# Performance work log

Measured on AMD Instinct MI355X. Metric: run time of the kernel, lower is better.

Reference implementation:

```python
import jax, jax.numpy as jnp
import numpy as np


def log_g(x):
    # log of g(x) = x+0.5 if x>=0 else sigmoid(x)
    return jnp.where(x >= 0, jnp.log(jax.nn.relu(x) + 0.5), -jax.nn.softplus(-x))


def setup_inputs() -> dict:
    key = jax.random.key(0)
    B, T, D, H = 8, 4096, 1024, 1024
    ks = jax.random.split(key, 7)
    s = 1.0 / np.sqrt(D)
    return {
        "x": jax.random.normal(ks[0], (B, T, D), dtype=jnp.float32),
        "h0": jnp.zeros((B, 1, H), dtype=jnp.float32),
        "W_f": jax.random.uniform(ks[1], (H, D), jnp.float32, -s, s),
        "b_f": jax.random.uniform(ks[2], (H,), jnp.float32, -s, s),
        "W_i": jax.random.uniform(ks[3], (H, D), jnp.float32, -s, s),
        "b_i": jax.random.uniform(ks[4], (H,), jnp.float32, -s, s),
        "W_h": jax.random.uniform(ks[5], (H, D), jnp.float32, -s, s),
        "b_h": jax.random.uniform(ks[6], (H,), jnp.float32, -s, s),
    }


def reference(x, h0, W_f, b_f, W_i, b_i, W_h, b_h):
    # gate pre-activations: [B, T, H]
    zf = jnp.einsum("btd,hd->bth", x, W_f) + b_f
    zi = jnp.einsum("btd,hd->bth", x, W_i) + b_i
    zh = jnp.einsum("btd,hd->bth", x, W_h) + b_h
    diff = jax.nn.softplus(-zf) - jax.nn.softplus(-zi)
    log_f = -jax.nn.softplus(diff)        # log f'_t
    log_i = -jax.nn.softplus(-diff)       # log i'_t
    log_values = jnp.concatenate([log_g(h0), log_i + log_g(zh)], axis=1)  # [B, T+1, H]
    # parallel scan in log space
    a_star = jnp.pad(jnp.cumsum(log_f, axis=1), ((0, 0), (1, 0), (0, 0)))  # [B, T+1, H]
    log_h = a_star + jax.lax.cumlogsumexp(log_values - a_star, axis=1)
    return jnp.exp(log_h)[:, 1:]  # [B, T, H]
```

## Files before the change

### kernel.cpp

```cpp
#include <hip/hip_runtime.h>
#include <hip/hip_bf16.h>
#include <stdint.h>
#include <stddef.h>

#define B_ 8
#define T_ 4096
#define D_ 1024
#define H_ 1024
#define M_ (B_*T_)
#define N_ 3072
#define K_ 1024
#define CHUNK 64
#define NCHUNK 64
#define NWG ((M_/256)*(N_/256))

typedef __attribute__((ext_vector_type(8))) __bf16 bf16v8;
typedef __attribute__((ext_vector_type(4))) float f32x4;
typedef __attribute__((ext_vector_type(8))) unsigned short u16x8;

#define REG_SZ 16384
#define SLOT_SZ 32768
#define BOFF 65536
#define LDS_BYTES 131072

#define FENCE() asm volatile("" ::: "memory")
#define SBAR()  __builtin_amdgcn_s_barrier()

__device__ __forceinline__ unsigned short f2bf(float f) {
  union { float f; unsigned u; } x; x.f = f;
  return (unsigned short)((x.u + 0x7fffu + ((x.u >> 16) & 1u)) >> 16);
}

__global__ __launch_bounds__(256) void cvt_x(const float* __restrict__ src,
                                             unsigned short* __restrict__ dst) {
  int i = blockIdx.x * 256 + threadIdx.x;
  const float4* s = (const float4*)src;
  float4 a = s[i*2], b = s[i*2+1];
  u16x8 o;
  o[0]=f2bf(a.x); o[1]=f2bf(a.y); o[2]=f2bf(a.z); o[3]=f2bf(a.w);
  o[4]=f2bf(b.x); o[5]=f2bf(b.y); o[6]=f2bf(b.z); o[7]=f2bf(b.w);
  *(u16x8*)(dst + (size_t)i*8) = o;
}

__global__ __launch_bounds__(256) void cvt_w(const float* __restrict__ w0,
                                             const float* __restrict__ w1,
                                             const float* __restrict__ w2,
                                             unsigned short* __restrict__ dst) {
  int i = blockIdx.x * 256 + threadIdx.x;
  int seg = i >> 17;
  int off = i & 131071;
  const float* src = (seg == 0) ? w0 : (seg == 1) ? w1 : w2;
  const float4* s = (const float4*)src;
  float4 a = s[off*2], b = s[off*2+1];
  u16x8 o;
  o[0]=f2bf(a.x); o[1]=f2bf(a.y); o[2]=f2bf(a.z); o[3]=f2bf(a.w);
  o[4]=f2bf(b.x); o[5]=f2bf(b.y); o[6]=f2bf(b.z); o[7]=f2bf(b.w);
  *(u16x8*)(dst + (size_t)i*8) = o;
}

__device__ __forceinline__ void stage_half(int k, int m0, int n0,
    const unsigned short* Abf, const unsigned short* Bbf, char* smem, int tid) {
  if (k > 63) return;
  int t = k >> 2, w = k & 3;
  int q   = (w >= 2) ? 1 : 0;
  int isA = (w == 0 || w == 3);
  int slot = t & 1;
  int k0 = t * 64;
  const unsigned short* gbase = isA ? (Abf + (size_t)(m0 + q*128) * K_)
                                    : (Bbf + (size_t)(n0 + q*128) * K_);
  char* lbase = smem + (isA ? 0 : BOFF) + slot*SLOT_SZ + q*REG_SZ;
  #pragma unroll
  for (int l = 0; l < 2; ++l) {
    int o = tid*16 + l*8192;
    int row = o >> 7, cb = o & 127;
    int scb = cb ^ ((row & 7) << 4);
    const unsigned short* g = gbase + (size_t)row * K_ + k0 + (scb >> 1);
    __builtin_amdgcn_global_load_lds((const __attribute__((address_space(1))) void*)g,
        (__attribute__((address_space(3))) void*)(lbase + o), 16, 0, 0);
  }
}

__device__ __forceinline__ bf16v8 ldsA(const char* smem, int slot, int q, int rr, int cb) {
  return *(const bf16v8*)(smem + slot*SLOT_SZ + q*REG_SZ + rr*128 + (cb ^ ((rr & 7) << 4)));
}
__device__ __forceinline__ bf16v8 ldsB(const char* smem, int slot, int q, int rr, int cb) {
  return *(const bf16v8*)(smem + BOFF + slot*SLOT_SZ + q*REG_SZ + rr*128 + (cb ^ ((rr & 7) << 4)));
}

__global__ __launch_bounds__(512, 2) void gemm_gates(
    const unsigned short* __restrict__ Abf,
    const unsigned short* __restrict__ Bbf,
    const float* __restrict__ bf_, const float* __restrict__ bi_,
    const float* __restrict__ bh_,
    float* __restrict__ zf, float* __restrict__ zi, float* __restrict__ zh)
{
  extern __shared__ char smem[];
  int tid = threadIdx.x;
  int bid = blockIdx.x;
  int swz = (bid & 7) * (NWG/8) + (bid >> 3);
  int tn = swz % 12, tm = swz / 12;
  int m0 = tm*256, n0 = tn*256;
  int lane = tid & 63, wid = tid >> 6;
  int wm = wid >> 2, wn = wid & 3;
  int lr = lane & 15, lhi = lane >> 4;
  int cbL = lhi * 16;

  f32x4 acc[8][4] = {};
  bf16v8 a0[4][2], b0[2][2], b1[2][2];

  #pragma unroll
  for (int k = 0; k < 7; ++k) stage_half(k, m0, n0, Abf, Bbf, smem, tid);
  asm volatile("s_waitcnt vmcnt(6)" ::: "memory");
  SBAR(); FENCE();

  for (int t = 0; t < 16; ++t) {
    int slot = t & 1;
    #pragma unroll
    for (int i = 0; i < 4; ++i)
      #pragma unroll
      for (int kk = 0; kk < 2; ++kk)
        a0[i][kk] = ldsA(smem, slot, 0, wm*64 + i*16 + lr, kk*64 + cbL);
    #pragma unroll
    for (int j = 0; j < 2; ++j)
      #pragma unroll
      for (int kk = 0; kk < 2; ++kk)
        b0[j][kk] = ldsB(smem, slot, 0, wn*32 + j*16 + lr, kk*64 + cbL);
    stage_half(4*t + 7, m0, n0, Abf, Bbf, smem, tid);
    FENCE(); SBAR(); FENCE();
    __builtin_amdgcn_s_setprio(1);
    #pragma unroll
    for (int i = 0; i < 4; ++i)
      #pragma unroll
      for (int j = 0; j < 2; ++j)
        #pragma unroll
        for (int kk = 0; kk < 2; ++kk)
          acc[i][j] = __builtin_amdgcn_mfma_f32_16x16x32_bf16(a0[i][kk], b0[j][kk], acc[i][j], 0, 0, 0);
    __builtin_amdgcn_s_setprio(0);
    FENCE(); SBAR(); FENCE();
    #pragma unroll
    for (int j = 0; j < 2; ++j)
      #pragma unroll
      for (int kk = 0; kk < 2; ++kk)
        b1[j][kk] = ldsB(smem, slot, 1, wn*32 + j*16 + lr, kk*64 + cbL);
    stage_half(4*t + 8, m0, n0, Abf, Bbf, smem, tid);
    FENCE(); SBAR(); FENCE();
    __builtin_amdgcn_s_setprio(1);
    #pragma unroll
    for (int i = 0; i < 4; ++i)
      #pragma unroll
      for (int j = 0; j < 2; ++j)
        #pragma unroll
        for (int kk = 0; kk < 2; ++kk)
          acc[i][2+j] = __builtin_amdgcn_mfma_f32_16x16x32_bf16(a0[i][kk], b1[j][kk], acc[i][2+j], 0, 0, 0);
    __builtin_amdgcn_s_setprio(0);
    FENCE(); SBAR(); FENCE();
    #pragma unroll
    for (int i = 0; i < 4; ++i)
      #pragma unroll
      for (int kk = 0; kk < 2; ++kk)
        a0[i][kk] = ldsA(smem, slot, 1, wm*64 + i*16 + lr, kk*64 + cbL);
    stage_half(4*t + 9, m0, n0, Abf, Bbf, smem, tid);
    FENCE(); SBAR(); FENCE();
    __builtin_amdgcn_s_setprio(1);
    #pragma unroll
    for (int i = 0; i < 4; ++i)
      #pragma unroll
      for (int j = 0; j < 2; ++j)
        #pragma unroll
        for (int kk = 0; kk < 2; ++kk)
          acc[4+i][2+j] = __builtin_amdgcn_mfma_f32_16x16x32_bf16(a0[i][kk], b1[j][kk], acc[4+i][2+j], 0, 0, 0);
    __builtin_amdgcn_s_setprio(0);
    FENCE(); SBAR(); FENCE();
    stage_half(4*t + 10, m0, n0, Abf, Bbf, smem, tid);
    FENCE(); SBAR(); FENCE();
    __builtin_amdgcn_s_setprio(1);
    #pragma unroll
    for (int i = 0; i < 4; ++i)
      #pragma unroll
      for (int j = 0; j < 2; ++j)
        #pragma unroll
        for (int kk = 0; kk < 2; ++kk)
          acc[4+i][j] = __builtin_amdgcn_mfma_f32_16x16x32_bf16(a0[i][kk], b0[j][kk], acc[4+i][j], 0, 0, 0);
    __builtin_amdgcn_s_setprio(0);
    if (t < 14) { asm volatile("s_waitcnt vmcnt(6)" ::: "memory"); }
    else        { asm volatile("s_waitcnt vmcnt(0)" ::: "memory"); }
    SBAR(); FENCE();
  }

  int g = n0 >> 10;
  float* Z = (g == 0) ? zf : (g == 1) ? zi : zh;
  const float* bias = (g == 0) ? bf_ : (g == 1) ? bi_ : bh_;
  int ncol0 = n0 & 1023;
  #pragma unroll
  for (int qm = 0; qm < 2; ++qm)
    #pragma unroll
    for (int i = 0; i < 4; ++i)
      #pragma unroll
      for (int qn = 0; qn < 2; ++qn)
        #pragma unroll
        for (int j = 0; j < 2; ++j) {
          int col = ncol0 + qn*128 + wn*32 + j*16 + lr;
          float bv = bias[col];
          int row = m0 + qm*128 + wm*64 + i*16 + lhi*4;
          f32x4 a = acc[qm*4+i][qn*2+j];
          #pragma unroll
          for (int r = 0; r < 4; ++r)
            Z[(size_t)(row + r)*H_ + col] = a[r] + bv;
        }
}

__device__ __forceinline__ void gate_eval(float vzf, float vzi, float vzh,
                                          float& f, float& v) {
  float spf = fmaxf(-vzf, 0.f) + __logf(1.f + __expf(-fabsf(vzf)));
  float spi = fmaxf(-vzi, 0.f) + __logf(1.f + __expf(-fabsf(vzi)));
  float d   = spf - spi;
  float l1  = __logf(1.f + __expf(-fabsf(d)));
  f = __expf(-(fmaxf(d, 0.f) + l1));
  float iv = __expf(-(fmaxf(-d, 0.f) + l1));
  float gv = (vzh >= 0.f) ? (vzh + 0.5f) : 1.f/(1.f + __expf(-vzh));
  v = iv * gv;
}

__global__ __launch_bounds__(256) void scan_phaseA(
    const float* zf, const float* __restrict__ zi,
    const float* __restrict__ zh, uint32_t* fv,
    float* __restrict__ Aw, float* __restrict__ Sw)
{
  int blk = blockIdx.x;
  int c = blk & 63, b = blk >> 6;
  int h4 = threadIdx.x * 4;
  size_t base = ((size_t)b*T_ + (size_t)c*CHUNK)*H_ + h4;
  float Ap[4] = {1.f,1.f,1.f,1.f}, S[4] = {0.f,0.f,0.f,0.f};
  for (int t = 0; t < CHUNK; ++t) {
    size_t idx = base + (size_t)t*H_;
    float4 vf = *(const float4*)(zf + idx);
    float4 vi = *(const float4*)(zi + idx);
    float4 vh = *(const float4*)(zh + idx);
    uint32_t o[4];
    const float* pf = (const float*)&vf;
    const float* pi = (const float*)&vi;
    const float* ph = (const float*)&vh;
    #pragma unroll
    for (int u = 0; u < 4; ++u) {
      float f, v;
      gate_eval(pf[u], pi[u], ph[u], f, v);
      o[u] = (uint32_t)f2bf(f) | ((uint32_t)f2bf(v) << 16);
      S[u] = fmaf(f, S[u], v);
      Ap[u] *= f;
    }
    uint4 ov; ov.x = o[0]; ov.y = o[1]; ov.z = o[2]; ov.w = o[3];
    *(uint4*)(fv + idx) = ov;
  }
  size_t widx = ((size_t)b*NCHUNK + c)*H_ + h4;
  *(float4*)(Aw + widx) = make_float4(Ap[0], Ap[1], Ap[2], Ap[3]);
  *(float4*)(Sw + widx) = make_float4(S[0], S[1], S[2], S[3]);
}

__global__ __launch_bounds__(256) void scan_phaseB(
    const float* __restrict__ Aw, const float* __restrict__ Sw,
    const float* __restrict__ h0, float* __restrict__ Cw)
{
  int i = blockIdx.x*256 + threadIdx.x;
  int b = i >> 8;
  int h4 = (i & 255) * 4;
  float4 x0 = *(const float4*)(h0 + (size_t)b*H_ + h4);
  float run[4];
  const float* px = (const float*)&x0;
  #pragma unroll
  for (int u = 0; u < 4; ++u)
    run[u] = (px[u] >= 0.f) ? (px[u] + 0.5f) : 1.f/(1.f + __expf(-px[u]));
  for (int c = 0; c < NCHUNK; ++c) {
    size_t idx = ((size_t)b*NCHUNK + c)*H_ + h4;
    *(float4*)(Cw + idx) = make_float4(run[0], run[1], run[2], run[3]);
    float4 av = *(const float4*)(Aw + idx);
    float4 sv = *(const float4*)(Sw + idx);
    const float* pa = (const float*)&av;
    const float* ps = (const float*)&sv;
    #pragma unroll
    for (int u = 0; u < 4; ++u) run[u] = fmaf(pa[u], run[u], ps[u]);
  }
}

__global__ __launch_bounds__(256) void scan_phaseC(
    const uint32_t* __restrict__ fv, const float* __restrict__ Cw,
    float* __restrict__ out)
{
  int blk = blockIdx.x;
  int c = blk & 63, b = blk >> 6;
  int h4 = threadIdx.x * 4;
  float4 cw = *(const float4*)(Cw + ((size_t)b*NCHUNK + c)*H_ + h4);
  float hh[4];
  const float* pc = (const float*)&cw;
  #pragma unroll
  for (int u = 0; u < 4; ++u) hh[u] = pc[u];
  size_t base = ((size_t)b*T_ + (size_t)c*CHUNK)*H_ + h4;
  for (int t = 0; t < CHUNK; ++t) {
    size_t idx = base + (size_t)t*H_;
    uint4 pk = *(const uint4*)(fv + idx);
    uint32_t w[4] = {pk.x, pk.y, pk.z, pk.w};
    #pragma unroll
    for (int u = 0; u < 4; ++u) {
      union { uint32_t u; float f; } cf, cv;
      cf.u = (w[u] & 0xffffu) << 16;
      cv.u = w[u] & 0xffff0000u;
      hh[u] = fmaf(cf.f, hh[u], cv.f);
    }
    *(float4*)(out + idx) = make_float4(hh[0], hh[1], hh[2], hh[3]);
  }
}

extern "C" void kernel_launch(void* const* d_in, const int* in_sizes, int n_in,
                              void* d_out, int out_size, void* d_ws, size_t ws_size,
                              hipStream_t stream) {
  const float* x   = (const float*)d_in[0];
  const float* h0  = (const float*)d_in[1];
  const float* W_f = (const float*)d_in[2];
  const float* b_f = (const float*)d_in[3];
  const float* W_i = (const float*)d_in[4];
  const float* b_i = (const float*)d_in[5];
  const float* W_h = (const float*)d_in[6];
  const float* b_h = (const float*)d_in[7];
  float* out = (float*)d_out;

  char* ws = (char*)d_ws;
  unsigned short* xb = (unsigned short*)ws;
  unsigned short* Wc = (unsigned short*)(ws + (size_t)M_*K_*2);
  float* zf = (float*)(ws + (size_t)M_*K_*2 + (size_t)N_*K_*2);
  float* zi = zf + (size_t)M_*H_;
  float* Aw = zi + (size_t)M_*H_;
  float* Sw = Aw + (size_t)B_*NCHUNK*H_;
  float* Cw = Sw + (size_t)B_*NCHUNK*H_;
  float* zh = out;
  uint32_t* fv = (uint32_t*)zf;

  static int smem_set = 0;
  (void)hipFuncSetAttribute((const void*)gemm_gates,
      hipFuncAttributeMaxDynamicSharedMemorySize, LDS_BYTES);
  (void)smem_set;

  cvt_x<<<M_*K_/8/256, 256, 0, stream>>>(x, xb);
  cvt_w<<<3*H_*K_/8/256, 256, 0, stream>>>(W_f, W_i, W_h, Wc);

  gemm_gates<<<NWG, 512, LDS_BYTES, stream>>>(xb, Wc, b_f, b_i, b_h, zf, zi, zh);

  scan_phaseA<<<B_*NCHUNK, 256, 0, stream>>>(zf, zi, zh, fv, Aw, Sw);
  scan_phaseB<<<B_*H_/4/256, 256, 0, stream>>>(Aw, Sw, h0, Cw);
  scan_phaseC<<<B_*NCHUNK, 256, 0, stream>>>(fv, Cw, out);
}
```

Measured before the change: 626.4 us.

## Fuse gate activations into GEMM epilogue with per-tile f/i/h weight blocks

```diff
diff --git a/kernel.cpp b/kernel.cpp
--- a/kernel.cpp
+++ b/kernel.cpp
@@ -8,19 +8,20 @@
 #define D_ 1024
 #define H_ 1024
 #define M_ (B_*T_)
-#define N_ 3072
 #define K_ 1024
 #define CHUNK 64
 #define NCHUNK 64
-#define NWG ((M_/256)*(N_/256))
+#define NWGF ((M_/128)*(H_/128))
 
 typedef __attribute__((ext_vector_type(8))) __bf16 bf16v8;
 typedef __attribute__((ext_vector_type(4))) float f32x4;
 typedef __attribute__((ext_vector_type(8))) unsigned short u16x8;
 
-#define REG_SZ 16384
-#define SLOT_SZ 32768
-#define BOFF 65536
+#define QA  0
+#define QBF 16384
+#define QBI 32768
+#define QBH 49152
+#define SLOT 65536
 #define LDS_BYTES 131072
 
 #define FENCE() asm volatile("" ::: "memory")
@@ -58,17 +59,8 @@
   *(u16x8*)(dst + (size_t)i*8) = o;
 }
 
-__device__ __forceinline__ void stage_half(int k, int m0, int n0,
-    const unsigned short* Abf, const unsigned short* Bbf, char* smem, int tid) {
-  if (k > 63) return;
-  int t = k >> 2, w = k & 3;
-  int q   = (w >= 2) ? 1 : 0;
-  int isA = (w == 0 || w == 3);
-  int slot = t & 1;
-  int k0 = t * 64;
-  const unsigned short* gbase = isA ? (Abf + (size_t)(m0 + q*128) * K_)
-                                    : (Bbf + (size_t)(n0 + q*128) * K_);
-  char* lbase = smem + (isA ? 0 : BOFF) + slot*SLOT_SZ + q*REG_SZ;
+__device__ __forceinline__ void stage_mat(char* lbase, const unsigned short* gbase,
+                                          int k0, int tid) {
   #pragma unroll
   for (int l = 0; l < 2; ++l) {
     int o = tid*16 + l*8192;
@@ -80,133 +72,8 @@
   }
 }
 
-__device__ __forceinline__ bf16v8 ldsA(const char* smem, int slot, int q, int rr, int cb) {
-  return *(const bf16v8*)(smem + slot*SLOT_SZ + q*REG_SZ + rr*128 + (cb ^ ((rr & 7) << 4)));
-}
-__device__ __forceinline__ bf16v8 ldsB(const char* smem, int slot, int q, int rr, int cb) {
-  return *(const bf16v8*)(smem + BOFF + slot*SLOT_SZ + q*REG_SZ + rr*128 + (cb ^ ((rr & 7) << 4)));
-}
-
-__global__ __launch_bounds__(512, 2) void gemm_gates(
-    const unsigned short* __restrict__ Abf,
-    const unsigned short* __restrict__ Bbf,
-    const float* __restrict__ bf_, const float* __restrict__ bi_,
-    const float* __restrict__ bh_,
-    float* __restrict__ zf, float* __restrict__ zi, float* __restrict__ zh)
-{
-  extern __shared__ char smem[];
-  int tid = threadIdx.x;
-  int bid = blockIdx.x;
-  int swz = (bid & 7) * (NWG/8) + (bid >> 3);
-  int tn = swz % 12, tm = swz / 12;
-  int m0 = tm*256, n0 = tn*256;
-  int lane = tid & 63, wid = tid >> 6;
-  int wm = wid >> 2, wn = wid & 3;
-  int lr = lane & 15, lhi = lane >> 4;
-  int cbL = lhi * 16;
-
-  f32x4 acc[8][4] = {};
-  bf16v8 a0[4][2], b0[2][2], b1[2][2];
-
-  #pragma unroll
-  for (int k = 0; k < 7; ++k) stage_half(k, m0, n0, Abf, Bbf, smem, tid);
-  asm volatile("s_waitcnt vmcnt(6)" ::: "memory");
-  SBAR(); FENCE();
-
-  for (int t = 0; t < 16; ++t) {
-    int slot = t & 1;
-    #pragma unroll
-    for (int i = 0; i < 4; ++i)
-      #pragma unroll
-      for (int kk = 0; kk < 2; ++kk)
-        a0[i][kk] = ldsA(smem, slot, 0, wm*64 + i*16 + lr, kk*64 + cbL);
-    #pragma unroll
-    for (int j = 0; j < 2; ++j)
-      #pragma unroll
-      for (int kk = 0; kk < 2; ++kk)
-        b0[j][kk] = ldsB(smem, slot, 0, wn*32 + j*16 + lr, kk*64 + cbL);
-    stage_half(4*t + 7, m0, n0, Abf, Bbf, smem, tid);
-    FENCE(); SBAR(); FENCE();
-    __builtin_amdgcn_s_setprio(1);
-    #pragma unroll
-    for (int i = 0; i < 4; ++i)
-      #pragma unroll
-      for (int j = 0; j < 2; ++j)
-        #pragma unroll
-        for (int kk = 0; kk < 2; ++kk)
-          acc[i][j] = __builtin_amdgcn_mfma_f32_16x16x32_bf16(a0[i][kk], b0[j][kk], acc[i][j], 0, 0, 0);
-    __builtin_amdgcn_s_setprio(0);
-    FENCE(); SBAR(); FENCE();
-    #pragma unroll
-    for (int j = 0; j < 2; ++j)
-      #pragma unroll
-      for (int kk = 0; kk < 2; ++kk)
-        b1[j][kk] = ldsB(smem, slot, 1, wn*32 + j*16 + lr, kk*64 + cbL);
-    stage_half(4*t + 8, m0, n0, Abf, Bbf, smem, tid);
-    FENCE(); SBAR(); FENCE();
-    __builtin_amdgcn_s_setprio(1);
-    #pragma unroll
-    for (int i = 0; i < 4; ++i)
-      #pragma unroll
-      for (int j = 0; j < 2; ++j)
-        #pragma unroll
-        for (int kk = 0; kk < 2; ++kk)
-          acc[i][2+j] = __builtin_amdgcn_mfma_f32_16x16x32_bf16(a0[i][kk], b1[j][kk], acc[i][2+j], 0, 0, 0);
-    __builtin_amdgcn_s_setprio(0);
-    FENCE(); SBAR(); FENCE();
-    #pragma unroll
-    for (int i = 0; i < 4; ++i)
-      #pragma unroll
-      for (int kk = 0; kk < 2; ++kk)
-        a0[i][kk] = ldsA(smem, slot, 1, wm*64 + i*16 + lr, kk*64 + cbL);
-    stage_half(4*t + 9, m0, n0, Abf, Bbf, smem, tid);
-    FENCE(); SBAR(); FENCE();
-    __builtin_amdgcn_s_setprio(1);
-    #pragma unroll
-    for (int i = 0; i < 4; ++i)
-      #pragma unroll
-      for (int j = 0; j < 2; ++j)
-        #pragma unroll
-        for (int kk = 0; kk < 2; ++kk)
-          acc[4+i][2+j] = __builtin_amdgcn_mfma_f32_16x16x32_bf16(a0[i][kk], b1[j][kk], acc[4+i][2+j], 0, 0, 0);
-    __builtin_amdgcn_s_setprio(0);
-    FENCE(); SBAR(); FENCE();
-    stage_half(4*t + 10, m0, n0, Abf, Bbf, smem, tid);
-    FENCE(); SBAR(); FENCE();
-    __builtin_amdgcn_s_setprio(1);
-    #pragma unroll
-    for (int i = 0; i < 4; ++i)
-      #pragma unroll
-      for (int j = 0; j < 2; ++j)
-        #pragma unroll
-        for (int kk = 0; kk < 2; ++kk)
-          acc[4+i][j] = __builtin_amdgcn_mfma_f32_16x16x32_bf16(a0[i][kk], b0[j][kk], acc[4+i][j], 0, 0, 0);
-    __builtin_amdgcn_s_setprio(0);
-    if (t < 14) { asm volatile("s_waitcnt vmcnt(6)" ::: "memory"); }
-    else        { asm volatile("s_waitcnt vmcnt(0)" ::: "memory"); }
-    SBAR(); FENCE();
-  }
-
-  int g = n0 >> 10;
-  float* Z = (g == 0) ? zf : (g == 1) ? zi : zh;
-  const float* bias = (g == 0) ? bf_ : (g == 1) ? bi_ : bh_;
-  int ncol0 = n0 & 1023;
-  #pragma unroll
-  for (int qm = 0; qm < 2; ++qm)
-    #pragma unroll
-    for (int i = 0; i < 4; ++i)
-      #pragma unroll
-      for (int qn = 0; qn < 2; ++qn)
-        #pragma unroll
-        for (int j = 0; j < 2; ++j) {
-          int col = ncol0 + qn*128 + wn*32 + j*16 + lr;
-          float bv = bias[col];
-          int row = m0 + qm*128 + wm*64 + i*16 + lhi*4;
-          f32x4 a = acc[qm*4+i][qn*2+j];
-          #pragma unroll
-          for (int r = 0; r < 4; ++r)
-            Z[(size_t)(row + r)*H_ + col] = a[r] + bv;
-        }
+__device__ __forceinline__ bf16v8 ldsRd(const char* base, int rr, int cb) {
+  return *(const bf16v8*)(base + rr*128 + (cb ^ ((rr & 7) << 4)));
 }
 
 __device__ __forceinline__ void gate_eval(float vzf, float vzi, float vzh,
@@ -221,9 +88,133 @@
   v = iv * gv;
 }
 
+__global__ __launch_bounds__(512, 2) void gemm_fused(
+    const unsigned short* __restrict__ Abf,
+    const unsigned short* __restrict__ Wc,
+    const float* __restrict__ bf_, const float* __restrict__ bi_,
+    const float* __restrict__ bh_,
+    uint32_t* __restrict__ fv)
+{
+  extern __shared__ char smem[];
+  int tid = threadIdx.x;
+  int bid = blockIdx.x;
+  int swz = (bid & 7) * (NWGF/8) + (bid >> 3);
+  int tn = swz & 7, tm = swz >> 3;
+  int m0 = tm*128, n0 = tn*128;
+  int lane = tid & 63, wid = tid >> 6;
+  int wm = wid >> 2, wn = wid & 3;
+  int lr = lane & 15, lhi = lane >> 4;
+  int cbL = lhi * 16;
+
+  const unsigned short* Ag  = Abf + (size_t)m0 * K_;
+  const unsigned short* BFg = Wc + (size_t)n0 * K_;
+  const unsigned short* BIg = Wc + (size_t)(H_ + n0) * K_;
+  const unsigned short* BHg = Wc + (size_t)(2*H_ + n0) * K_;
+
+  f32x4 accF[4][2] = {}, accI[4][2] = {}, accH[4][2] = {};
+  bf16v8 af[4][2], bF[2][2], bI[2][2], bH[2][2];
+
+  stage_mat(smem + QA,  Ag,  0, tid);
+  stage_mat(smem + QBF, BFg, 0, tid);
+  stage_mat(smem + QBI, BIg, 0, tid);
+  stage_mat(smem + QBH, BHg, 0, tid);
+  asm volatile("s_waitcnt vmcnt(4)" ::: "memory");
+  SBAR(); FENCE();
+
+  for (int t = 0; t < 16; ++t) {
+    char* rd = smem + (t & 1)*SLOT;
+    char* wr = smem + ((t & 1) ^ 1)*SLOT;
+    int k1 = (t+1)*64;
+    bool st = (t < 15);
+    #pragma unroll
+    for (int i = 0; i < 4; ++i)
+      #pragma unroll
+      for (int kk = 0; kk < 2; ++kk)
+        af[i][kk] = ldsRd(rd + QA, wm*64 + i*16 + lr, kk*64 + cbL);
+    #pragma unroll
+    for (int j = 0; j < 2; ++j)
+      #pragma unroll
+      for (int kk = 0; kk < 2; ++kk)
+        bF[j][kk] = ldsRd(rd + QBF, wn*32 + j*16 + lr, kk*64 + cbL);
+    if (st) { stage_mat(wr + QA, Ag, k1, tid); stage_mat(wr + QBF, BFg, k1, tid); }
+    FENCE();
+    __builtin_amdgcn_s_setprio(1);
+    #pragma unroll
+    for (int i = 0; i < 4; ++i)
+      #pragma unroll
+      for (int j = 0; j < 2; ++j)
+        #pragma unroll
+        for (int kk = 0; kk < 2; ++kk)
+          accF[i][j] = __builtin_amdgcn_mfma_f32_16x16x32_bf16(af[i][kk], bF[j][kk], accF[i][j], 0, 0, 0);
+    __builtin_amdgcn_s_setprio(0);
+    FENCE();
+    if (st) { asm volatile("s_waitcnt vmcnt(6)" ::: "memory"); }
+    else    { asm volatile("s_waitcnt vmcnt(2)" ::: "memory"); }
+    SBAR(); FENCE();
+    #pragma unroll
+    for (int j = 0; j < 2; ++j)
+      #pragma unroll
+      for (int kk = 0; kk < 2; ++kk)
+        bI[j][kk] = ldsRd(rd + QBI, wn*32 + j*16 + lr, kk*64 + cbL);
+    if (st) stage_mat(wr + QBI, BIg, k1, tid);
+    FENCE();
+    __builtin_amdgcn_s_setprio(1);
+    #pragma unroll
+    for (int i = 0; i < 4; ++i)
+      #pragma unroll
+      for (int j = 0; j < 2; ++j)
+        #pragma unroll
+        for (int kk = 0; kk < 2; ++kk)
+          accI[i][j] = __builtin_amdgcn_mfma_f32_16x16x32_bf16(af[i][kk], bI[j][kk], accI[i][j], 0, 0, 0);
+    __builtin_amdgcn_s_setprio(0);
+    FENCE();
+    if (st) { asm volatile("s_waitcnt vmcnt(6)" ::: "memory"); }
+    else    { asm volatile("s_waitcnt vmcnt(0)" ::: "memory"); }
+    SBAR(); FENCE();
+    #pragma unroll
+    for (int j = 0; j < 2; ++j)
+      #pragma unroll
+      for (int kk = 0; kk < 2; ++kk)
+        bH[j][kk] = ldsRd(rd + QBH, wn*32 + j*16 + lr, kk*64 + cbL);
+    if (st) stage_mat(wr + QBH, BHg, k1, tid);
+    FENCE();
+    __builtin_amdgcn_s_setprio(1);
+    #pragma unroll
+    for (int i = 0; i < 4; ++i)
+      #pragma unroll
+      for (int j = 0; j < 2; ++j)
+        #pragma unroll
+        for (int kk = 0; kk < 2; ++kk)
+          accH[i][j] = __builtin_amdgcn_mfma_f32_16x16x32_bf16(af[i][kk], bH[j][kk], accH[i][j], 0, 0, 0);
+    __builtin_amdgcn_s_setprio(0);
+    if (st) { asm volatile("s_waitcnt vmcnt(4)" ::: "memory"); SBAR(); FENCE(); }
+  }
+
+  float bfv[2], biv[2], bhv[2];
+  #pragma unroll
+  for (int j = 0; j < 2; ++j) {
+    int col = n0 + wn*32 + j*16 + lr;
+    bfv[j] = bf_[col]; biv[j] = bi_[col]; bhv[j] = bh_[col];
+  }
+  #pragma unroll
+  for (int i = 0; i < 4; ++i)
+    #pragma unroll
+    for (int j = 0; j < 2; ++j) {
+      int col = n0 + wn*32 + j*16 + lr;
+      int row0 = m0 + wm*64 + i*16 + lhi*4;
+      #pragma unroll
+      for (int r = 0; r < 4; ++r) {
+        float f, v;
+        gate_eval(accF[i][j][r] + bfv[j], accI[i][j][r] + biv[j],
+                  accH[i][j][r] + bhv[j], f, v);
+        fv[(size_t)(row0 + r)*H_ + col] =
+            (uint32_t)f2bf(f) | ((uint32_t)f2bf(v) << 16);
+      }
+    }
+}
+
 __global__ __launch_bounds__(256) void scan_phaseA(
-    const float* zf, const float* __restrict__ zi,
-    const float* __restrict__ zh, uint32_t* fv,
+    const uint32_t* __restrict__ fv,
     float* __restrict__ Aw, float* __restrict__ Sw)
 {
   int blk = blockIdx.x;
@@ -232,24 +223,16 @@
   size_t base = ((size_t)b*T_ + (size_t)c*CHUNK)*H_ + h4;
   float Ap[4] = {1.f,1.f,1.f,1.f}, S[4] = {0.f,0.f,0.f,0.f};
   for (int t = 0; t < CHUNK; ++t) {
-    size_t idx = base + (size_t)t*H_;
-    float4 vf = *(const float4*)(zf + idx);
-    float4 vi = *(const float4*)(zi + idx);
-    float4 vh = *(const float4*)(zh + idx);
-    uint32_t o[4];
-    const float* pf = (const float*)&vf;
-    const float* pi = (const float*)&vi;
-    const float* ph = (const float*)&vh;
+    uint4 pk = *(const uint4*)(fv + base + (size_t)t*H_);
+    uint32_t w[4] = {pk.x, pk.y, pk.z, pk.w};
     #pragma unroll
     for (int u = 0; u < 4; ++u) {
-      float f, v;
-      gate_eval(pf[u], pi[u], ph[u], f, v);
-      o[u] = (uint32_t)f2bf(f) | ((uint32_t)f2bf(v) << 16);
-      S[u] = fmaf(f, S[u], v);
-      Ap[u] *= f;
+      union { uint32_t u; float f; } cf, cv;
+      cf.u = (w[u] & 0xffffu) << 16;
+      cv.u = w[u] & 0xffff0000u;
+      S[u] = fmaf(cf.f, S[u], cv.f);
+      Ap[u] *= cf.f;
     }
-    uint4 ov; ov.x = o[0]; ov.y = o[1]; ov.z = o[2]; ov.w = o[3];
-    *(uint4*)(fv + idx) = ov;
   }
   size_t widx = ((size_t)b*NCHUNK + c)*H_ + h4;
   *(float4*)(Aw + widx) = make_float4(Ap[0], Ap[1], Ap[2], Ap[3]);
@@ -325,25 +308,20 @@
   char* ws = (char*)d_ws;
   unsigned short* xb = (unsigned short*)ws;
   unsigned short* Wc = (unsigned short*)(ws + (size_t)M_*K_*2);
-  float* zf = (float*)(ws + (size_t)M_*K_*2 + (size_t)N_*K_*2);
-  float* zi = zf + (size_t)M_*H_;
-  float* Aw = zi + (size_t)M_*H_;
+  uint32_t* fv = (uint32_t*)(ws + (size_t)M_*K_*2 + (size_t)3*H_*K_*2);
+  float* Aw = (float*)(fv + (size_t)M_*H_);
   float* Sw = Aw + (size_t)B_*NCHUNK*H_;
   float* Cw = Sw + (size_t)B_*NCHUNK*H_;
-  float* zh = out;
-  uint32_t* fv = (uint32_t*)zf;
-
-  static int smem_set = 0;
-  (void)hipFuncSetAttribute((const void*)gemm_gates,
+
+  (void)hipFuncSetAttribute((const void*)gemm_fused,
       hipFuncAttributeMaxDynamicSharedMemorySize, LDS_BYTES);
-  (void)smem_set;
 
   cvt_x<<<M_*K_/8/256, 256, 0, stream>>>(x, xb);
   cvt_w<<<3*H_*K_/8/256, 256, 0, stream>>>(W_f, W_i, W_h, Wc);
 
-  gemm_gates<<<NWG, 512, LDS_BYTES, stream>>>(xb, Wc, b_f, b_i, b_h, zf, zi, zh);
-
-  scan_phaseA<<<B_*NCHUNK, 256, 0, stream>>>(zf, zi, zh, fv, Aw, Sw);
+  gemm_fused<<<NWGF, 512, LDS_BYTES, stream>>>(xb, Wc, b_f, b_i, b_h, fv);
+
+  scan_phaseA<<<B_*NCHUNK, 256, 0, stream>>>(fv, Aw, Sw);
   scan_phaseB<<<B_*H_/4/256, 256, 0, stream>>>(Aw, Sw, h0, Cw);
   scan_phaseC<<<B_*NCHUNK, 256, 0, stream>>>(fv, Cw, out);
 }
```

Result: faster. 567.5 us (-9.4%).
